# Kernel optimization log

Hardware: AMD Instinct MI355X
Metric: run time of the kernel (lower is better)

## Reference

```python
import jax, jax.numpy as jnp
import numpy as np

H, DK, NHID, L, G = 8, 32, 256, 2, 16
SQRT_DK = float(np.sqrt(DK))
N_IN = (3, 3, 2)  # number of etypes whose dst is word, topic, doc (for mean cross-reducer)


def _seg_softmax_agg(a, val, dst, n):
    # per-destination-node softmax over incoming edges (DGL mailbox softmax), then weighted sum
    m = jax.ops.segment_max(a, dst, num_segments=n)
    m = jnp.where(m < -1e30, 0.0, m)  # empty segments
    ex = jnp.exp(a - m[dst])
    den = jax.ops.segment_sum(ex, dst, num_segments=n)
    w = ex / jnp.maximum(den, 1e-9)[dst]
    return jax.ops.segment_sum(w[..., None] * val, dst, num_segments=n)  # [n,H,DK]


def _forward(word_id, topic_id, g_word, g_topic, g_doc,
             src_ww, dst_ww, src_wd, dst_wd, src_wt, dst_wt, src_td, dst_td, src_tt, dst_tt,
             time_ww, time_wd, time_wt, time_td, y_data,
             word_embeds, topic_embeds, doc_gen, adapt_w, adapt_b,
             time_tab, time_w, time_b,
             kW, kB, qW, qB, vW, vB, aW, aB, skip, ln_g, ln_b,
             pri, attR, msgR, out_w, out_b):
    nd = g_doc.shape[0]
    # initial node features: word via adapt_ws, topic lookup, doc broadcast
    h = [word_embeds[word_id] @ adapt_w + adapt_b,
         topic_embeds[topic_id],
         jnp.tile(doc_gen, (nd, 1))]
    te = lambda t: time_tab[t] @ time_w + time_b  # RelTemporalEncoding: lin(emb(t)) -> [E, DK]
    th_ww, th_wd, th_wt, th_td = te(time_ww), te(time_wd), te(time_wt), te(time_td)
    # etype index order: wt, wd, td, tt, ww, tw, dt, dw ; ntype index: 0=word,1=topic,2=doc
    rels = [(0, 0, 1, src_wt, dst_wt, th_wt), (1, 0, 2, src_wd, dst_wd, th_wd),
            (2, 1, 2, src_td, dst_td, th_td), (3, 1, 1, src_tt, dst_tt, None),
            (4, 0, 0, src_ww, dst_ww, th_ww), (5, 1, 0, dst_wt, src_wt, th_wt),
            (6, 2, 1, dst_td, src_td, th_td), (7, 2, 0, dst_wd, src_wd, th_wd)]
    for li in range(L):
        k = [(h[i] @ kW[li, i] + kB[li, i]).reshape(-1, H, DK) for i in range(3)]
        q = [(h[i] @ qW[li, i] + qB[li, i]).reshape(-1, H, DK) for i in range(3)]
        v = [(h[i] @ vW[li, i] + vB[li, i]).reshape(-1, H, DK) for i in range(3)]
        t = [jnp.zeros((h[i].shape[0], NHID), h[i].dtype) for i in range(3)]
        for (e, s, d, src, dst, th) in rels:
            key = jnp.einsum('ehk,hkl->ehl', k[s][src], attR[li, e])
            a = (q[d][dst] * key).sum(-1) * pri[li, e] / SQRT_DK  # [E,H]
            val = jnp.einsum('ehk,hkl->ehl', v[s][src], msgR[li, e])
            if th is not None:
                val = val + th[:, None, :]  # temporal encoding broadcast over heads
            n = h[d].shape[0]
            he = _seg_softmax_agg(a, val, dst, n)
            t[d] = t[d] + jax.nn.relu(he.reshape(n, NHID))  # relu per etype, then mean
        nh = []
        for i in range(3):
            alpha = jax.nn.sigmoid(skip[li, i])
            trans = (t[i] / N_IN[i]) @ aW[li, i] + aB[li, i]
            out = trans * alpha + h[i] * (1.0 - alpha)
            mu = out.mean(-1, keepdims=True)
            var = ((out - mu) ** 2).mean(-1, keepdims=True)
            nh.append((out - mu) / jnp.sqrt(var + 1e-5) * ln_g[li, i] + ln_b[li, i])
        h = nh
    gmax = lambda x, g: jax.ops.segment_max(x, g, num_segments=G)  # dgl.max_nodes
    gi = jnp.concatenate([gmax(h[2], g_doc), gmax(h[0], g_word), gmax(h[1], g_topic)], -1)
    logits = gi @ out_w + out_b  # [G,1]
    z = logits.reshape(-1)
    loss = jnp.mean(jnp.maximum(z, 0.0) - z * y_data + jnp.log1p(jnp.exp(-jnp.abs(z))))
    return loss, jax.nn.sigmoid(logits)


def setup_inputs():
    key = jax.random.key(0)
    ks = iter(jax.random.split(key, 80))
    nrm = lambda shape, s=0.05: jax.random.normal(next(ks), shape, jnp.float32) * s
    ri = lambda shape, hi: jax.random.randint(next(ks), shape, 0, hi)
    NW, NT, ND = 30000, 2000, 8000
    d = {}
    d['word_id'] = ri((NW,), 15000)
    d['topic_id'] = ri((NT,), 50)
    d['g_word'] = jnp.sort(ri((NW,), G))
    d['g_topic'] = jnp.sort(ri((NT,), G))
    d['g_doc'] = jnp.sort(ri((ND,), G))
    d['src_ww'] = ri((40000,), NW); d['dst_ww'] = ri((40000,), NW); d['time_ww'] = ri((40000,), 7)
    d['src_wd'] = ri((30000,), NW); d['dst_wd'] = ri((30000,), ND); d['time_wd'] = ri((30000,), 7)
    d['src_wt'] = ri((30000,), NW); d['dst_wt'] = ri((30000,), NT); d['time_wt'] = ri((30000,), 7)
    d['src_td'] = ri((25000,), NT); d['dst_td'] = ri((25000,), ND); d['time_td'] = ri((25000,), 7)
    d['src_tt'] = ri((20000,), NT); d['dst_tt'] = ri((20000,), NT)
    d['y_data'] = jax.random.uniform(next(ks), (G,), jnp.float32)
    d['word_embeds'] = nrm((15000, 256))
    d['topic_embeds'] = nrm((50, 256), 0.1)
    d['doc_gen'] = nrm((1, 256), 0.1)
    d['adapt_w'] = nrm((256, 256)); d['adapt_b'] = nrm((256,), 0.01)
    d['time_tab'] = nrm((7, 32), 0.1); d['time_w'] = nrm((32, 32), 0.1); d['time_b'] = nrm((32,), 0.01)
    for nm in ['kW', 'qW', 'vW', 'aW']:
        d[nm] = nrm((L, 3, 256, 256))
    for nm in ['kB', 'qB', 'vB', 'aB']:
        d[nm] = nrm((L, 3, 256), 0.01)
    d['skip'] = jnp.ones((L, 3))
    d['ln_g'] = jnp.ones((L, 3, 256)); d['ln_b'] = jnp.zeros((L, 3, 256))
    d['pri'] = jnp.ones((L, 8, H))
    d['attR'] = nrm((L, 8, H, DK, DK), 0.1)
    d['msgR'] = nrm((L, 8, H, DK, DK), 0.1)
    d['out_w'] = nrm((3 * NHID, 1)); d['out_b'] = jnp.zeros((1,))
    return d


def reference(word_id, topic_id, g_word, g_topic, g_doc,
              src_ww, dst_ww, time_ww, src_wd, dst_wd, time_wd,
              src_wt, dst_wt, time_wt, src_td, dst_td, time_td,
              src_tt, dst_tt, y_data,
              word_embeds, topic_embeds, doc_gen, adapt_w, adapt_b,
              time_tab, time_w, time_b,
              kW, kB, qW, qB, vW, vB, aW, aB, skip, ln_g, ln_b,
              pri, attR, msgR, out_w, out_b):
    return _forward(word_id, topic_id, g_word, g_topic, g_doc,
                    src_ww, dst_ww, src_wd, dst_wd, src_wt, dst_wt, src_td, dst_td, src_tt, dst_tt,
                    time_ww, time_wd, time_wt, time_td, y_data,
                    word_embeds, topic_embeds, doc_gen, adapt_w, adapt_b,
                    time_tab, time_w, time_b,
                    kW, kB, qW, qB, vW, vB, aW, aB, skip, ln_g, ln_b,
                    pri, attR, msgR, out_w, out_b)
```

## Files before the change

### kernel.cpp

```cpp
#include <hip/hip_runtime.h>
#include <hip/hip_bf16.h>
#include <math.h>

#define H 8
#define DK 32
#define NHID 256
#define LNUM 2
#define GNUM 16

typedef float f32x4 __attribute__((ext_vector_type(4)));
typedef short bf16x8 __attribute__((ext_vector_type(8)));
typedef unsigned short u16x8 __attribute__((ext_vector_type(8)));

__device__ __forceinline__ unsigned encf(float f) {
    unsigned u = __float_as_uint(f);
    return (u & 0x80000000u) ? ~u : (u | 0x80000000u);
}
__device__ __forceinline__ float decf(unsigned u) {
    return __uint_as_float((u & 0x80000000u) ? (u ^ 0x80000000u) : ~u);
}
__device__ __forceinline__ float bfd(unsigned short u) {
    return __uint_as_float(((unsigned)u) << 16);
}
__device__ __forceinline__ unsigned short f2bf(float x) {
    __hip_bfloat16 b = __float2bfloat16(x);
    return *reinterpret_cast<unsigned short*>(&b);
}

#define APAN2(row, kb) ((((kb) >> 7) << 12) + ((row) << 6) + ((((kb) & 127) ^ (((row) & 7) << 4)) >> 1))
__device__ __forceinline__ size_t swzA(int row, int col ) {
    return (((size_t)(row >> 6)) << 14) + (size_t)APAN2(row & 63, col * 2);
}
#define SWZB(row, kb)  (((row) << 6) + ((((kb) ^ (((row) & 7) << 4))) >> 1))

struct CsrArgs  { const int* dst[8]; const int* srcA[8]; const int* timA[8];
                  int relOfs[9]; int dstBase[8]; };
struct BdAllArgs{ int rows[8]; int srcOfs[8]; int outOfs[8]; };
struct Ek1PosArgs{ int kOfs[8]; int qOfs[8]; };
struct Ek3AllArgs{ int dstBase[8]; int vOfs[8]; int hasTim[8]; int typeRel[9]; int nrT[3];
                   int cumN[4]; int tOfs[3]; float oScale[3]; };
struct GmaxArgs { const float* hp[3]; const int* grp[3]; int n[3]; int colBase[3]; };
struct GBArgs   { int rb[4]; int nLoc[3]; int li3; };
struct MLArgs   { int rowOfs[4]; int nLoc[3]; int li3; };

__global__ void te_kernel(const float* __restrict__ time_tab, const float* __restrict__ time_w,
                          const float* __restrict__ time_b, float* __restrict__ te7) {
    int t = threadIdx.x >> 5, j = threadIdx.x & 31;
    if (t < 7) {
        float s = time_b[j];
        #pragma unroll
        for (int i = 0; i < 32; ++i) s += time_tab[t * 32 + i] * time_w[i * 32 + j];
        te7[t * 32 + j] = s;
    }
}

__global__ void gather_rows(const float* __restrict__ emb, const int* __restrict__ idx,
                            float* __restrict__ out, unsigned short* __restrict__ outB, int n) {
    int row = blockIdx.x, c = threadIdx.x;
    if (row < n) {
        float v = emb[(size_t)idx[row] * 256 + c];
        out[(size_t)row * 256 + c] = v;
        outB[swzA(row, c)] = f2bf(v);
    }
}

__global__ void bcast_row(const float* __restrict__ src, float* __restrict__ out,
                          unsigned short* __restrict__ outB, int n) {
    int row = blockIdx.x, c = threadIdx.x;
    if (row < n) {
        float v = src[c];
        out[(size_t)row * 256 + c] = v;
        outB[swzA(row, c)] = f2bf(v);
    }
}

__global__ __launch_bounds__(256) void wtr_kernel(
    const float* __restrict__ adaptW, const float* __restrict__ kW, const float* __restrict__ qW,
    const float* __restrict__ vW, const float* __restrict__ aW, unsigned short* __restrict__ WT) {
    int z = blockIdx.z;
    const float* src;
    if (z == 0) src = adaptW;
    else if (z < 7)  src = kW + (size_t)(z - 1) * 65536;
    else if (z < 13) src = qW + (size_t)(z - 7) * 65536;
    else if (z < 19) src = vW + (size_t)(z - 13) * 65536;
    else             src = aW + (size_t)(z - 19) * 65536;
    unsigned short* dst = WT + (size_t)z * 65536;
    __shared__ float tile[32][33];
    int tx = threadIdx.x & 31, ty = threadIdx.x >> 5;
    int kb = blockIdx.x * 32, cb = blockIdx.y * 32;
    #pragma unroll
    for (int i = 0; i < 4; ++i)
        tile[ty + i * 8][tx] = src[(size_t)(kb + ty + i * 8) * 256 + cb + tx];
    __syncthreads();
    #pragma unroll
    for (int i = 0; i < 4; ++i) {
        int col = cb + ty + i * 8, k = kb + tx;
        dst[((col >> 6) * 4 + (k >> 6)) * 4096 + SWZB(col & 63, (k & 63) * 2)] =
            f2bf(tile[tx][ty + i * 8]);
    }
}

__global__ __launch_bounds__(256) void gemm_batch(
    const unsigned short* __restrict__ Apan,
    const unsigned short* __restrict__ WT, int wBase, int nz,
    const float* __restrict__ b0, const float* __restrict__ b1, const float* __restrict__ b2,
    void* __restrict__ o0, void* __restrict__ o1, void* __restrict__ o2,
    int outBf16, GBArgs ga)
{
    __shared__ unsigned short As[64 * 256];
    __shared__ unsigned short Bs[2][4096];
    const int tid = threadIdx.x;
    const int lane = tid & 63, wv = tid >> 6;
    const int b = blockIdx.x;
    const int t = (b >= ga.rb[2]) ? 2 : ((b >= ga.rb[1]) ? 1 : 0);
    const int nLoc = ga.nLoc[t];
    const int locRowBase = (b - ga.rb[t]) * 64;
    const int cb6 = blockIdx.y;
    const int mBase = wBase + ga.li3 + t;
    {
        const u16x8* src = reinterpret_cast<const u16x8*>(Apan + (((size_t)b) << 14));
        u16x8* dst = reinterpret_cast<u16x8*>(As);
        #pragma unroll
        for (int it = 0; it < 8; ++it)
            dst[it * 256 + tid] = src[it * 256 + tid];
    }
    const int fr = lane & 15, fg = lane >> 4;
    const int wrow = (wv & 1) * 32, wcol = (wv >> 1) * 32;
    const int nt = nz * 4;
    {
        const u16x8* src = reinterpret_cast<const u16x8*>(WT + (size_t)mBase * 65536 + (size_t)(cb6 * 4 + 0) * 4096);
        u16x8* dst = reinterpret_cast<u16x8*>(Bs[0]);
        dst[tid] = src[tid];
        dst[tid + 256] = src[tid + 256];
    }
    __syncthreads();

    f32x4 acc[2][2];
    #pragma unroll
    for (int m = 0; m < 2; ++m)
        #pragma unroll
        for (int nn = 0; nn < 2; ++nn) acc[m][nn] = 0.f;

    for (int tt2 = 0; tt2 < nt; ++tt2) {
        const int cur = tt2 & 1;
        const int ks = tt2 & 3, z = tt2 >> 2;
        u16x8 w0, w1;
        const bool pf = (tt2 + 1 < nt);
        if (pf) {
            int tn = tt2 + 1;
            const u16x8* src = reinterpret_cast<const u16x8*>(
                WT + (size_t)(mBase + (tn >> 2) * 6) * 65536 + (size_t)(cb6 * 4 + (tn & 3)) * 4096);
            w0 = src[tid];
            w1 = src[tid + 256];
        }
        #pragma unroll
        for (int kk = 0; kk < 2; ++kk) {
            bf16x8 af0 = *reinterpret_cast<bf16x8*>(&As[APAN2(wrow + fr,      ks * 128 + kk * 64 + fg * 16)]);
            bf16x8 af1 = *reinterpret_cast<bf16x8*>(&As[APAN2(wrow + 16 + fr, ks * 128 + kk * 64 + fg * 16)]);
            bf16x8 bf0 = *reinterpret_cast<bf16x8*>(&Bs[cur][SWZB(wcol + fr,      kk * 64 + fg * 16)]);
            bf16x8 bf1 = *reinterpret_cast<bf16x8*>(&Bs[cur][SWZB(wcol + 16 + fr, kk * 64 + fg * 16)]);
            acc[0][0] = __builtin_amdgcn_mfma_f32_16x16x32_bf16(af0, bf0, acc[0][0], 0, 0, 0);
            acc[0][1] = __builtin_amdgcn_mfma_f32_16x16x32_bf16(af0, bf1, acc[0][1], 0, 0, 0);
            acc[1][0] = __builtin_amdgcn_mfma_f32_16x16x32_bf16(af1, bf0, acc[1][0], 0, 0, 0);
            acc[1][1] = __builtin_amdgcn_mfma_f32_16x16x32_bf16(af1, bf1, acc[1][1], 0, 0, 0);
        }
        if (pf) {
            u16x8* dst = reinterpret_cast<u16x8*>(Bs[cur ^ 1]);
            dst[tid] = w0;
            dst[tid + 256] = w1;
        }
        if (ks == 3) {
            const float* biasB = (z == 0) ? b0 : ((z == 1) ? b1 : b2);
            const float* bias = biasB + (size_t)(ga.li3 + t) * 256;
            void* outp = (z == 0) ? o0 : ((z == 1) ? o1 : o2);
            #pragma unroll
            for (int m = 0; m < 2; ++m) {
                #pragma unroll
                for (int r = 0; r < 4; ++r) {
                    int lr = locRowBase + wrow + m * 16 + fg * 4 + r;
                    if (lr >= nLoc) continue;
                    size_t gr = (size_t)b * 64 + wrow + m * 16 + fg * 4 + r;
                    #pragma unroll
                    for (int nn = 0; nn < 2; ++nn) {
                        int gc = cb6 * 64 + wcol + nn * 16 + fr;
                        float v = acc[m][nn][r] + bias[gc];
                        if (outBf16) ((unsigned short*)outp)[gr * 256 + gc] = f2bf(v);
                        else         ((float*)outp)[gr * 256 + gc] = v;
                    }
                }
            }
            #pragma unroll
            for (int m = 0; m < 2; ++m)
                #pragma unroll
                for (int nn = 0; nn < 2; ++nn) acc[m][nn] = 0.f;
        }
        __syncthreads();
    }
}

__global__ __launch_bounds__(256) void gemm_init(
    const float* __restrict__ A, const int* __restrict__ gidx,
    const unsigned short* __restrict__ WT, const float* __restrict__ bias,
    float* __restrict__ outF, unsigned short* __restrict__ dupB, int n)
{
    __shared__ unsigned short As[64 * 256];
    __shared__ unsigned short Bs[2][4096];
    const int tid = threadIdx.x;
    const int lane = tid & 63, wv = tid >> 6;
    const int rowBase = blockIdx.x * 64;
    const int cb6 = blockIdx.y;
    #pragma unroll 4
    for (int it = 0; it < 16; ++it) {
        int row = it * 4 + wv;
        int r = rowBase + row;
        ushort4 p = make_ushort4(0, 0, 0, 0);
        if (r < n) {
            int ar = gidx[r];
            float4 v = *reinterpret_cast<const float4*>(A + (size_t)ar * 256 + lane * 4);
            p.x = f2bf(v.x); p.y = f2bf(v.y); p.z = f2bf(v.z); p.w = f2bf(v.w);
        }
        *reinterpret_cast<ushort4*>(&As[APAN2(row, lane * 8)]) = p;
    }
    const int fr = lane & 15, fg = lane >> 4;
    const int wrow = (wv & 1) * 32, wcol = (wv >> 1) * 32;
    {
        const u16x8* src = reinterpret_cast<const u16x8*>(WT + (size_t)(cb6 * 4 + 0) * 4096);
        u16x8* dst = reinterpret_cast<u16x8*>(Bs[0]);
        dst[tid] = src[tid];
        dst[tid + 256] = src[tid + 256];
    }
    __syncthreads();
    f32x4 acc[2][2];
    #pragma unroll
    for (int m = 0; m < 2; ++m)
        #pragma unroll
        for (int nn = 0; nn < 2; ++nn) acc[m][nn] = 0.f;
    for (int t = 0; t < 4; ++t) {
        const int cur = t & 1;
        u16x8 w0, w1;
        const bool pf = (t + 1 < 4);
        if (pf) {
            const u16x8* src = reinterpret_cast<const u16x8*>(WT + (size_t)(cb6 * 4 + t + 1) * 4096);
            w0 = src[tid];
            w1 = src[tid + 256];
        }
        #pragma unroll
        for (int kk = 0; kk < 2; ++kk) {
            bf16x8 af0 = *reinterpret_cast<bf16x8*>(&As[APAN2(wrow + fr,      t * 128 + kk * 64 + fg * 16)]);
            bf16x8 af1 = *reinterpret_cast<bf16x8*>(&As[APAN2(wrow + 16 + fr, t * 128 + kk * 64 + fg * 16)]);
            bf16x8 bf0 = *reinterpret_cast<bf16x8*>(&Bs[cur][SWZB(wcol + fr,      kk * 64 + fg * 16)]);
            bf16x8 bf1 = *reinterpret_cast<bf16x8*>(&Bs[cur][SWZB(wcol + 16 + fr, kk * 64 + fg * 16)]);
            acc[0][0] = __builtin_amdgcn_mfma_f32_16x16x32_bf16(af0, bf0, acc[0][0], 0, 0, 0);
            acc[0][1] = __builtin_amdgcn_mfma_f32_16x16x32_bf16(af0, bf1, acc[0][1], 0, 0, 0);
            acc[1][0] = __builtin_amdgcn_mfma_f32_16x16x32_bf16(af1, bf0, acc[1][0], 0, 0, 0);
            acc[1][1] = __builtin_amdgcn_mfma_f32_16x16x32_bf16(af1, bf1, acc[1][1], 0, 0, 0);
        }
        if (pf) {
            u16x8* dst = reinterpret_cast<u16x8*>(Bs[cur ^ 1]);
            dst[tid] = w0;
            dst[tid + 256] = w1;
        }
        __syncthreads();
    }
    #pragma unroll
    for (int m = 0; m < 2; ++m) {
        #pragma unroll
        for (int r = 0; r < 4; ++r) {
            int gr = rowBase + wrow + m * 16 + fg * 4 + r;
            if (gr >= n) continue;
            #pragma unroll
            for (int nn = 0; nn < 2; ++nn) {
                int gc = cb6 * 64 + wcol + nn * 16 + fr;
                float v = acc[m][nn][r] + bias[gc];
                outF[(size_t)gr * 256 + gc] = v;
                dupB[swzA(gr, gc)] = f2bf(v);
            }
        }
    }
}

__global__ __launch_bounds__(256) void bd_all(
    const unsigned short* __restrict__ inPb, const float* __restrict__ Rl,
    const float* __restrict__ priL, int isV,
    unsigned short* __restrict__ outAll, BdAllArgs A)
{
    const int rel = blockIdx.z;
    const int n = A.rows[rel];
    const int rowBase = blockIdx.x * 128;
    if (rowBase >= n) return;
    const unsigned short* in = inPb + (size_t)A.srcOfs[rel] * 256;
    const float* R = Rl + (size_t)rel * 8192;
    unsigned short* out = outAll + (size_t)A.outOfs[rel] * 256;
    const int head = blockIdx.y;
    const float oscale = isV ? 1.f : (priL[rel * 8 + head] * 0.17677669529663687f);
    const int tid = threadIdx.x, lane = tid & 63, wv = tid >> 6;
    const int fr = lane & 15, fg = lane >> 4;
    const float* Rh = R + head * 1024;
    bf16x8 b0, b1;
    #pragma unroll
    for (int j = 0; j < 8; ++j) {
        b0[j] = (short)f2bf(Rh[(fg * 8 + j) * 32 + fr] * oscale);
        b1[j] = (short)f2bf(Rh[(fg * 8 + j) * 32 + 16 + fr] * oscale);
    }
    const int r0 = rowBase + wv * 32 + fr;
    const int r1 = r0 + 16;
    const int rc0 = (r0 < n) ? r0 : n - 1;
    const int rc1 = (r1 < n) ? r1 : n - 1;
    bf16x8 a0 = *reinterpret_cast<const bf16x8*>(in + (size_t)rc0 * 256 + head * 32 + fg * 8);
    bf16x8 a1 = *reinterpret_cast<const bf16x8*>(in + (size_t)rc1 * 256 + head * 32 + fg * 8);
    f32x4 acc00 = 0.f, acc01 = 0.f, acc10 = 0.f, acc11 = 0.f;
    acc00 = __builtin_amdgcn_mfma_f32_16x16x32_bf16(a0, b0, acc00, 0, 0, 0);
    acc01 = __builtin_amdgcn_mfma_f32_16x16x32_bf16(a0, b1, acc01, 0, 0, 0);
    acc10 = __builtin_amdgcn_mfma_f32_16x16x32_bf16(a1, b0, acc10, 0, 0, 0);
    acc11 = __builtin_amdgcn_mfma_f32_16x16x32_bf16(a1, b1, acc11, 0, 0, 0);
    const int colB = head * 32 + fr;
    #pragma unroll
    for (int r = 0; r < 4; ++r) {
        int g0 = rowBase + wv * 32 + fg * 4 + r;
        if (g0 < n) {
            out[(size_t)g0 * 256 + colB]      = f2bf(acc00[r]);
            out[(size_t)g0 * 256 + colB + 16] = f2bf(acc01[r]);
        }
        int g1 = g0 + 16;
        if (g1 < n) {
            out[(size_t)g1 * 256 + colB]      = f2bf(acc10[r]);
            out[(size_t)g1 * 256 + colB + 16] = f2bf(acc11[r]);
        }
    }
}

__global__ __launch_bounds__(256) void ek1_pos(
    const unsigned short* __restrict__ qPb, const unsigned short* __restrict__ kattAll,
    const int* __restrict__ payload, const int* __restrict__ drel,
    float* __restrict__ alogC, Ek1PosArgs A, int totE)
{
    int gid = blockIdx.x * 256 + threadIdx.x;
    int p = gid >> 3, h = gid & 7;
    if (p >= totE) return;
    int dr = drel[p];
    int d = dr & 0xFFFFF, rel = dr >> 20;
    int s = payload[p] & 0xFFFF;
    const u16x8* q8 = reinterpret_cast<const u16x8*>(qPb + ((size_t)(A.qOfs[rel] + d)) * 256 + h * 32);
    const u16x8* k8 = reinterpret_cast<const u16x8*>(kattAll + ((size_t)(A.kOfs[rel] + s)) * 256 + h * 32);
    float a = 0.f;
    #pragma unroll
    for (int j = 0; j < 4; ++j) {
        u16x8 qv = q8[j], kv = k8[j];
        #pragma unroll
        for (int m = 0; m < 8; ++m) a += bfd(qv[m]) * bfd(kv[m]);
    }
    alogC[(size_t)p * 8 + h] = a;
}

__global__ __launch_bounds__(256) void ek3_all(
    const unsigned short* __restrict__ vmsgAll, const float* __restrict__ alogC,
    const int* __restrict__ rowptrAll, const int* __restrict__ payload,
    const float* __restrict__ te7, unsigned short* __restrict__ tB, Ek3AllArgs A)
{
    __shared__ float sTe[224];
    if (threadIdx.x < 224) sTe[threadIdx.x] = te7[threadIdx.x];
    __syncthreads();
    int wv = threadIdx.x >> 6, lane = threadIdx.x & 63;
    int dg = blockIdx.x * 4 + wv;
    if (dg >= A.cumN[3]) return;
    const int ty = (dg >= A.cumN[2]) ? 2 : ((dg >= A.cumN[1]) ? 1 : 0);
    const int d = dg - A.cumN[ty];
    const int bl = lane >> 3, hl = lane & 7;
    const int c = lane * 4, hq = lane >> 3;
    float t0 = 0.f, t1 = 0.f, t2 = 0.f, t3 = 0.f;
    const int nr = A.nrT[ty];
    for (int j = 0; j < nr; ++j) {
        const int rel = A.typeRel[ty * 3 + j];
        int base = A.dstBase[rel] + d;
        int beg = rowptrAll[base], end = rowptrAll[base + 1];
        if (beg == end) continue;
        const int useTim = A.hasTim[rel];
        int rO = A.vOfs[rel];
        float m = -INFINITY, den = 0.f;
        float a0 = 0.f, a1 = 0.f, a2 = 0.f, a3 = 0.f;
        for (int p0 = beg; p0 < end; p0 += 8) {
            int p = p0 + bl;
            bool valid = p < end;
            int pc = valid ? p : end - 1;
            float a = valid ? alogC[(size_t)pc * 8 + hl] : -INFINITY;
            int pk = payload[pc];
            int sS = pk & 0xFFFF, tT = pk >> 16;
            float bm = a;
            bm = fmaxf(bm, __shfl_xor(bm, 8));
            bm = fmaxf(bm, __shfl_xor(bm, 16));
            bm = fmaxf(bm, __shfl_xor(bm, 32));
            float bmA = __shfl(bm, hq);
            float mN = fmaxf(m, bmA);
            float sc = __expf(m - mN);
            den *= sc; a0 *= sc; a1 *= sc; a2 *= sc; a3 *= sc;
            m = mN;
            float mL = __shfl(mN, hl * 8);
            float ex = valid ? __expf(a - mL) : 0.f;
            float ds = ex;
            ds += __shfl_xor(ds, 8);
            ds += __shfl_xor(ds, 16);
            ds += __shfl_xor(ds, 32);
            den += __shfl(ds, hq);
            int nb = end - p0; if (nb > 8) nb = 8;
            for (int b = 0; b < nb; ++b) {
                float w = __shfl(ex, b * 8 + hq);
                int sB = __shfl(sS, b * 8);
                ushort4 v = *reinterpret_cast<const ushort4*>(vmsgAll + ((size_t)(rO + sB)) * 256 + c);
                float vx = bfd(v.x), vy = bfd(v.y), vz = bfd(v.z), vw = bfd(v.w);
                if (useTim) {
                    int tBt = __shfl(tT, b * 8);
                    const float* tp = &sTe[tBt * 32 + (c & 31)];
                    vx += tp[0]; vy += tp[1]; vz += tp[2]; vw += tp[3];
                }
                a0 += w * vx; a1 += w * vy; a2 += w * vz; a3 += w * vw;
            }
        }
        float inv = 1.f / fmaxf(den, 1e-9f);
        t0 += fmaxf(a0 * inv, 0.f); t1 += fmaxf(a1 * inv, 0.f);
        t2 += fmaxf(a2 * inv, 0.f); t3 += fmaxf(a3 * inv, 0.f);
    }
    float os = A.oScale[ty];
    ushort4 o;
    o.x = f2bf(t0 * os); o.y = f2bf(t1 * os);
    o.z = f2bf(t2 * os); o.w = f2bf(t3 * os);
    *reinterpret_cast<ushort4*>(tB + swzA(A.tOfs[ty] + d, c)) = o;
}

__global__ void count_all(CsrArgs A, int* __restrict__ cnt, int totE) {
    int gid = blockIdx.x * 256 + threadIdx.x;
    if (gid >= totE) return;
    int r = 0;
    while (gid >= A.relOfs[r + 1]) ++r;
    int e = gid - A.relOfs[r];
    atomicAdd(&cnt[A.dstBase[r] + A.dst[r][e]], 1);
}
__global__ __launch_bounds__(1024) void scan1_k(const int* __restrict__ cnt, int* __restrict__ part,
                                                int* __restrict__ bsum, int n) {
    __shared__ int buf[1024];
    int tid = threadIdx.x, gid = blockIdx.x * 1024 + tid;
    int x = (gid < n) ? cnt[gid] : 0;
    buf[tid] = x; __syncthreads();
    for (int off = 1; off < 1024; off <<= 1) {
        int y = (tid >= off) ? buf[tid - off] : 0;
        __syncthreads();
        buf[tid] += y;
        __syncthreads();
    }
    if (gid < n) part[gid] = buf[tid];
    if (tid == 1023) bsum[blockIdx.x] = buf[1023];
}
__global__ __launch_bounds__(256) void scan2_k(int* __restrict__ bsum, int nb) {
    __shared__ int buf[256];
    int tid = threadIdx.x;
    buf[tid] = (tid < nb) ? bsum[tid] : 0;
    __syncthreads();
    for (int off = 1; off < 256; off <<= 1) {
        int y = (tid >= off) ? buf[tid - off] : 0;
        __syncthreads();
        buf[tid] += y;
        __syncthreads();
    }
    if (tid < nb) bsum[tid] = buf[tid];
}
__global__ void scan3_k(const int* __restrict__ cnt, const int* __restrict__ part,
                        const int* __restrict__ bsum, int* __restrict__ rowptr,
                        int* __restrict__ cur, int n) {
    int gid = blockIdx.x * 256 + threadIdx.x;
    if (gid < n) {
        int b = gid >> 10;
        int add = (b > 0) ? bsum[b - 1] : 0;
        int inc = part[gid] + add;
        rowptr[gid + 1] = inc;
        cur[gid] = inc - cnt[gid];
    }
    if (gid == 0) rowptr[0] = 0;
}
__global__ void scatter_all(CsrArgs A, int* __restrict__ cur,
                            int* __restrict__ payload, int* __restrict__ drel, int totE) {
    int gid = blockIdx.x * 256 + threadIdx.x;
    if (gid >= totE) return;
    int r = 0;
    while (gid >= A.relOfs[r + 1]) ++r;
    int e = gid - A.relOfs[r];
    int d = A.dst[r][e];
    int p = atomicAdd(&cur[A.dstBase[r] + d], 1);
    int s = A.srcA[r][e];
    int t = A.timA[r] ? A.timA[r][e] : 0;
    payload[p] = s | (t << 16);
    drel[p] = d | (r << 20);
}

__global__ __launch_bounds__(256) void mix_ln_all(
    float* __restrict__ h, unsigned short* __restrict__ hB, const float* __restrict__ trans,
    const float* __restrict__ skipP, const float* __restrict__ g, const float* __restrict__ b,
    MLArgs M)
{
    int row = blockIdx.x;
    int t = (row >= M.rowOfs[2]) ? 2 : ((row >= M.rowOfs[1]) ? 1 : 0);
    int d = row - M.rowOfs[t];
    if (d >= M.nLoc[t]) return;
    int j = M.li3 + t;
    int c = threadIdx.x;
    float alpha = 1.f / (1.f + expf(-skipP[j]));
    size_t off = (size_t)row * 256 + c;
    float o = trans[off] * alpha + h[off] * (1.f - alpha);
    float s = o, ss = o * o;
    #pragma unroll
    for (int dd = 1; dd < 64; dd <<= 1) { s += __shfl_xor(s, dd); ss += __shfl_xor(ss, dd); }
    __shared__ float rS[4], rSS[4];
    int w = threadIdx.x >> 6, lane = threadIdx.x & 63;
    if (lane == 0) { rS[w] = s; rSS[w] = ss; }
    __syncthreads();
    float S = rS[0] + rS[1] + rS[2] + rS[3];
    float SS = rSS[0] + rSS[1] + rSS[2] + rSS[3];
    float mean = S * (1.f / 256.f);
    float var = fmaxf(SS * (1.f / 256.f) - mean * mean, 0.f);
    float rs = rsqrtf(var + 1e-5f);
    float v = (o - mean) * rs * g[(size_t)j * 256 + c] + b[(size_t)j * 256 + c];
    h[off] = v;
    hB[swzA(row, c)] = f2bf(v);
}

__global__ __launch_bounds__(256) void gmax_all(GmaxArgs A, unsigned* __restrict__ gi) {
    int ty = blockIdx.y;
    int n = A.n[ty];
    int r0 = blockIdx.x * 64;
    if (r0 >= n) return;
    int col = threadIdx.x;
    const float* hp = A.hp[ty];
    const int* grp = A.grp[ty];
    int cbase = A.colBase[ty];
    int rend = (r0 + 64 < n) ? r0 + 64 : n;
    int cur = grp[r0];
    float m = -INFINITY;
    for (int r = r0; r < rend; ++r) {
        int g = grp[r];
        if (g != cur) {
            atomicMax(&gi[cur * 768 + cbase + col], encf(m));
            cur = g; m = -INFINITY;
        }
        m = fmaxf(m, hp[(size_t)r * 256 + col]);
    }
    atomicMax(&gi[cur * 768 + cbase + col], encf(m));
}

__global__ void gi_init(unsigned* __restrict__ gi) {
    int i = blockIdx.x * 256 + threadIdx.x;
    if (i < 16 * 768) gi[i] = 0x007FFFFFu;
}

__global__ __launch_bounds__(1024) void final_k(const unsigned* __restrict__ gi,
                                                const float* __restrict__ out_w,
                                                const float* __restrict__ out_b,
                                                const float* __restrict__ y,
                                                float* __restrict__ out) {
    int w = threadIdx.x >> 6, lane = threadIdx.x & 63;
    float s = 0.f;
    for (int c = lane; c < 768; c += 64) s += decf(gi[w * 768 + c]) * out_w[c];
    #pragma unroll
    for (int d = 1; d < 64; d <<= 1) s += __shfl_xor(s, d);
    __shared__ float lloss[16];
    if (lane == 0) {
        float z = s + out_b[0];
        out[1 + w] = 1.f / (1.f + expf(-z));
        lloss[w] = fmaxf(z, 0.f) - z * y[w] + log1pf(expf(-fabsf(z)));
    }
    __syncthreads();
    if (threadIdx.x == 0) {
        float L = 0.f;
        for (int g2 = 0; g2 < 16; ++g2) L += lloss[g2];
        out[0] = L * (1.f / 16.f);
    }
}

extern "C" void kernel_launch(void* const* d_in, const int* in_sizes, int n_in,
                              void* d_out, int out_size, void* d_ws, size_t ws_size,
                              hipStream_t stream) {
    const int* word_id   = (const int*)d_in[0];
    const int* topic_id  = (const int*)d_in[1];
    const int* g_word    = (const int*)d_in[2];
    const int* g_topic   = (const int*)d_in[3];
    const int* g_doc     = (const int*)d_in[4];
    const int* src_ww = (const int*)d_in[5];  const int* dst_ww = (const int*)d_in[6];  const int* time_ww = (const int*)d_in[7];
    const int* src_wd = (const int*)d_in[8];  const int* dst_wd = (const int*)d_in[9];  const int* time_wd = (const int*)d_in[10];
    const int* src_wt = (const int*)d_in[11]; const int* dst_wt = (const int*)d_in[12]; const int* time_wt = (const int*)d_in[13];
    const int* src_td = (const int*)d_in[14]; const int* dst_td = (const int*)d_in[15]; const int* time_td = (const int*)d_in[16];
    const int* src_tt = (const int*)d_in[17]; const int* dst_tt = (const int*)d_in[18];
    const float* y_data      = (const float*)d_in[19];
    const float* word_embeds = (const float*)d_in[20];
    const float* topic_embeds= (const float*)d_in[21];
    const float* doc_gen     = (const float*)d_in[22];
    const float* adapt_w     = (const float*)d_in[23];
    const float* adapt_b     = (const float*)d_in[24];
    const float* time_tab    = (const float*)d_in[25];
    const float* time_w      = (const float*)d_in[26];
    const float* time_b      = (const float*)d_in[27];
    const float* kW = (const float*)d_in[28];
    const float* qW = (const float*)d_in[29];
    const float* vW = (const float*)d_in[30];
    const float* aW = (const float*)d_in[31];
    const float* kB = (const float*)d_in[32];
    const float* qB = (const float*)d_in[33];
    const float* vB = (const float*)d_in[34];
    const float* aB = (const float*)d_in[35];
    const float* skip = (const float*)d_in[36];
    const float* ln_g = (const float*)d_in[37];
    const float* ln_b = (const float*)d_in[38];
    const float* pri  = (const float*)d_in[39];
    const float* attR = (const float*)d_in[40];
    const float* msgR = (const float*)d_in[41];
    const float* out_w = (const float*)d_in[42];
    const float* out_b = (const float*)d_in[43];

    const int NW = in_sizes[0], NT = in_sizes[1], ND = in_sizes[4];
    const int E_ww = in_sizes[5], E_wd = in_sizes[8], E_wt = in_sizes[11],
              E_td = in_sizes[14], E_tt = in_sizes[17];
    const int nN[3] = {NW, NT, ND};
    const float invNin[3] = {1.f / 3.f, 1.f / 3.f, 1.f / 2.f};

    struct Rel { int e, s, d; const int* src; const int* dst; const int* tim; int E; };
    const Rel rels[8] = {
        {0, 0, 1, src_wt, dst_wt, time_wt, E_wt},
        {1, 0, 2, src_wd, dst_wd, time_wd, E_wd},
        {2, 1, 2, src_td, dst_td, time_td, E_td},
        {3, 1, 1, src_tt, dst_tt, nullptr, E_tt},
        {4, 0, 0, src_ww, dst_ww, time_ww, E_ww},
        {5, 1, 0, dst_wt, src_wt, time_wt, E_wt},
        {6, 2, 1, dst_td, src_td, time_td, E_td},
        {7, 2, 0, dst_wd, src_wd, time_wd, E_wd},
    };

    int relOfs[9]; relOfs[0] = 0;
    int dstBase[8]; int acc = 0;
    for (int r = 0; r < 8; ++r) { relOfs[r + 1] = relOfs[r] + rels[r].E; dstBase[r] = acc; acc += nN[rels[r].d]; }
    const int totE = relOfs[8], totD = acc;

    int relRowOfs[8], relRowsTot = 0, maxRelRows = 0;
    for (int r = 0; r < 8; ++r) {
        relRowOfs[r] = relRowsTot;
        relRowsTot += nN[rels[r].s];
        if (nN[rels[r].s] > maxRelRows) maxRelRows = nN[rels[r].s];
    }

    int nPad[3], rowOfsT[4];
    rowOfsT[0] = 0;
    for (int i = 0; i < 3; ++i) { nPad[i] = (nN[i] + 63) & ~63; rowOfsT[i + 1] = rowOfsT[i] + nPad[i]; }
    const int totPad = rowOfsT[3];

    float* base = (float*)d_ws;
    size_t off = 0;
    auto take = [&](size_t nElems) { float* p = base + off; off += (nElems + 63) & ~(size_t)63; return p; };
    float* hPbase = take((size_t)totPad * 256);
    unsigned short* hB = (unsigned short*)take((size_t)totPad * 128);
    unsigned short* tB = (unsigned short*)take((size_t)totPad * 128);
    unsigned short* kPb = (unsigned short*)take((size_t)totPad * 128);
    unsigned short* qPb = (unsigned short*)take((size_t)totPad * 128);
    unsigned short* vPb = (unsigned short*)take((size_t)totPad * 128);
    size_t arenaFloats = (size_t)relRowsTot * 128;
    if ((size_t)totPad * 256 > arenaFloats) arenaFloats = (size_t)totPad * 256;
    float* uni = take(arenaFloats);
    unsigned short* arena = (unsigned short*)uni;
    float* trans = uni;
    unsigned short* WT = (unsigned short*)take((size_t)25 * 32768);
    float* alogC = take((size_t)totE * 8);
    float* te7  = take(7 * 32);
    unsigned* gi = (unsigned*)take(16 * 768);
    int* cntAll = (int*)take(totD);
    int* part   = (int*)take(totD);
    int* bsum   = (int*)take(256);
    int* rowptrAll = (int*)take(totD + 1);
    int* curAll = (int*)take(totD);
    int* payload = (int*)take(totE);
    int* drel    = (int*)take(totE);
    (void)ws_size; (void)n_in; (void)out_size;

    te_kernel<<<1, 256, 0, stream>>>(time_tab, time_w, time_b, te7);
    {
        dim3 g(8, 8, 25);
        wtr_kernel<<<g, 256, 0, stream>>>(adapt_w, kW, qW, vW, aW, WT);
    }
    CsrArgs ca;
    for (int r = 0; r < 8; ++r) {
        ca.dst[r] = rels[r].dst; ca.srcA[r] = rels[r].src; ca.timA[r] = rels[r].tim;
        ca.dstBase[r] = dstBase[r];
    }
    for (int r = 0; r < 9; ++r) ca.relOfs[r] = relOfs[r];
    hipMemsetAsync(cntAll, 0, (size_t)totD * sizeof(int), stream);
    count_all<<<(totE + 255) / 256, 256, 0, stream>>>(ca, cntAll, totE);
    int nb = (totD + 1023) / 1024;
    scan1_k<<<nb, 1024, 0, stream>>>(cntAll, part, bsum, totD);
    scan2_k<<<1, 256, 0, stream>>>(bsum, nb);
    scan3_k<<<(totD + 255) / 256, 256, 0, stream>>>(cntAll, part, bsum, rowptrAll, curAll, totD);
    scatter_all<<<(totE + 255) / 256, 256, 0, stream>>>(ca, curAll, payload, drel, totE);
    gi_init<<<48, 256, 0, stream>>>(gi);

    {
        dim3 g((NW + 63) / 64, 4);
        gemm_init<<<g, 256, 0, stream>>>(word_embeds, word_id, WT, adapt_b, hPbase, hB, NW);
    }
    gather_rows<<<NT, 256, 0, stream>>>(topic_embeds, topic_id,
                                        hPbase + (size_t)rowOfsT[1] * 256,
                                        hB + (size_t)rowOfsT[1] * 256, NT);
    bcast_row<<<ND, 256, 0, stream>>>(doc_gen,
                                      hPbase + (size_t)rowOfsT[2] * 256,
                                      hB + (size_t)rowOfsT[2] * 256, ND);

    BdAllArgs ba;
    Ek1PosArgs e1;
    Ek3AllArgs e3;
    for (int r = 0; r < 8; ++r) {
        const Rel& R = rels[r];
        ba.rows[r] = nN[R.s];
        ba.srcOfs[r] = rowOfsT[R.s];
        ba.outOfs[r] = relRowOfs[r];
        e1.kOfs[r] = relRowOfs[r]; e1.qOfs[r] = rowOfsT[R.d];
        e3.dstBase[r] = dstBase[r]; e3.vOfs[r] = relRowOfs[r];
        e3.hasTim[r] = (R.tim != nullptr) ? 1 : 0;
    }
    const int typeRel[9] = {4, 5, 7, 0, 3, 6, 1, 2, 0};
    for (int i = 0; i < 9; ++i) e3.typeRel[i] = typeRel[i];
    e3.nrT[0] = 3; e3.nrT[1] = 3; e3.nrT[2] = 2;
    e3.cumN[0] = 0; e3.cumN[1] = NW; e3.cumN[2] = NW + NT; e3.cumN[3] = NW + NT + ND;
    for (int i = 0; i < 3; ++i) { e3.tOfs[i] = rowOfsT[i]; e3.oScale[i] = invNin[i]; }

    GBArgs gb;
    for (int i = 0; i < 4; ++i) gb.rb[i] = rowOfsT[i] / 64;
    for (int i = 0; i < 3; ++i) gb.nLoc[i] = nN[i];
    MLArgs ml;
    for (int i = 0; i < 4; ++i) ml.rowOfs[i] = rowOfsT[i];
    for (int i = 0; i < 3; ++i) ml.nLoc[i] = nN[i];

    const int totBlocks = totPad / 64;
    const int totD3 = NW + NT + ND;
    for (int li = 0; li < LNUM; ++li) {
        gb.li3 = li * 3; ml.li3 = li * 3;
        {
            dim3 g(totBlocks, 4);
            gemm_batch<<<g, 256, 0, stream>>>(hB, WT, 1, 3, kB, qB, vB,
                                              kPb, qPb, vPb, 1, gb);
        }
        {
            dim3 g((maxRelRows + 127) / 128, 8, 8);
            bd_all<<<g, 256, 0, stream>>>(kPb, attR + (size_t)li * 8 * 8192,
                                          pri + (size_t)li * 8 * 8, 0, arena, ba);
        }
        ek1_pos<<<((size_t)totE * 8 + 255) / 256, 256, 0, stream>>>(
            qPb, arena, payload, drel, alogC, e1, totE);
        {
            dim3 g((maxRelRows + 127) / 128, 8, 8);
            bd_all<<<g, 256, 0, stream>>>(vPb, msgR + (size_t)li * 8 * 8192,
                                          pri + (size_t)li * 8 * 8, 1, arena, ba);
        }
        ek3_all<<<(totD3 + 3) / 4, 256, 0, stream>>>(arena, alogC, rowptrAll, payload,
                                                     te7, tB, e3);
        {
            dim3 g(totBlocks, 4);
            gemm_batch<<<g, 256, 0, stream>>>(tB, WT, 19, 1, aB, aB, aB,
                                              trans, trans, trans, 0, gb);
        }
        mix_ln_all<<<totPad, 256, 0, stream>>>(hPbase, hB, trans, skip, ln_g, ln_b, ml);
    }

    GmaxArgs ga;
    ga.hp[0] = hPbase + (size_t)rowOfsT[2] * 256; ga.grp[0] = g_doc;   ga.n[0] = ND; ga.colBase[0] = 0;
    ga.hp[1] = hPbase;                             ga.grp[1] = g_word;  ga.n[1] = NW; ga.colBase[1] = 256;
    ga.hp[2] = hPbase + (size_t)rowOfsT[1] * 256; ga.grp[2] = g_topic; ga.n[2] = NT; ga.colBase[2] = 512;
    int maxN = NW > ND ? (NW > NT ? NW : NT) : (ND > NT ? ND : NT);
    dim3 gg((maxN + 63) / 64, 3);
    gmax_all<<<gg, 256, 0, stream>>>(ga, gi);
    final_k<<<1, 1024, 0, stream>>>(gi, out_w, out_b, y_data, (float*)d_out);
}
```

Baseline: 658.2 us.

## Split edge softmax normalization into separate pass before message aggregation

Adds a kernel that computes per-destination, per-head softmax max and denominator over incoming edges and rewrites the attention logits in place as normalized weights. The aggregation kernel then just takes a weighted sum of messages, with no online-softmax rescaling or shuffle reductions inside its edge loop. The aim is to shorten the latency-bound gather loop, at the price of an extra launch and a second read-modify-write pass over the logits.

```diff
diff --git a/kernel.cpp b/kernel.cpp
--- a/kernel.cpp
+++ b/kernel.cpp
@@ -37,6 +37,7 @@
                   int relOfs[9]; int dstBase[8]; };
 struct BdAllArgs{ int rows[8]; int srcOfs[8]; int outOfs[8]; };
 struct Ek1PosArgs{ int kOfs[8]; int qOfs[8]; };
+struct EkwArgs  { int dstBase[8]; int typeRel[9]; int nrT[3]; int cumN[4]; };
 struct Ek3AllArgs{ int dstBase[8]; int vOfs[8]; int hasTim[8]; int typeRel[9]; int nrT[3];
                    int cumN[4]; int tOfs[3]; float oScale[3]; };
 struct GmaxArgs { const float* hp[3]; const int* grp[3]; int n[3]; int colBase[3]; };
@@ -352,6 +353,52 @@
     alogC[(size_t)p * 8 + h] = a;
 }
 
+__global__ __launch_bounds__(256) void ekw_all(
+    float* __restrict__ alogC, const int* __restrict__ rowptrAll, EkwArgs A)
+{
+    int wv = threadIdx.x >> 6, lane = threadIdx.x & 63;
+    int dg = blockIdx.x * 4 + wv;
+    if (dg >= A.cumN[3]) return;
+    const int ty = (dg >= A.cumN[2]) ? 2 : ((dg >= A.cumN[1]) ? 1 : 0);
+    const int d = dg - A.cumN[ty];
+    const int bl = lane >> 3, hl = lane & 7;
+    const int nr = A.nrT[ty];
+    for (int j = 0; j < nr; ++j) {
+        const int rel = A.typeRel[ty * 3 + j];
+        int base = A.dstBase[rel] + d;
+        int beg = rowptrAll[base], end = rowptrAll[base + 1];
+        if (beg == end) continue;
+        float m = -INFINITY, den = 0.f;
+        for (int p0 = beg; p0 < end; p0 += 8) {
+            int p = p0 + bl;
+            bool valid = p < end;
+            float a = valid ? alogC[(size_t)(valid ? p : end - 1) * 8 + hl] : -INFINITY;
+            float bm = a;
+            bm = fmaxf(bm, __shfl_xor(bm, 8));
+            bm = fmaxf(bm, __shfl_xor(bm, 16));
+            bm = fmaxf(bm, __shfl_xor(bm, 32));
+            float mN = fmaxf(m, bm);
+            float sc = __expf(m - mN);
+            den *= sc;
+            float ex = valid ? __expf(a - mN) : 0.f;
+            float ds = ex;
+            ds += __shfl_xor(ds, 8);
+            ds += __shfl_xor(ds, 16);
+            ds += __shfl_xor(ds, 32);
+            den += ds;
+            m = mN;
+        }
+        float inv = 1.f / fmaxf(den, 1e-9f);
+        for (int p0 = beg; p0 < end; p0 += 8) {
+            int p = p0 + bl;
+            if (p < end) {
+                float a = alogC[(size_t)p * 8 + hl];
+                alogC[(size_t)p * 8 + hl] = __expf(a - m) * inv;
+            }
+        }
+    }
+}
+
 __global__ __launch_bounds__(256) void ek3_all(
     const unsigned short* __restrict__ vmsgAll, const float* __restrict__ alogC,
     const int* __restrict__ rowptrAll, const int* __restrict__ payload,
@@ -376,34 +423,17 @@
         if (beg == end) continue;
         const int useTim = A.hasTim[rel];
         int rO = A.vOfs[rel];
-        float m = -INFINITY, den = 0.f;
         float a0 = 0.f, a1 = 0.f, a2 = 0.f, a3 = 0.f;
         for (int p0 = beg; p0 < end; p0 += 8) {
             int p = p0 + bl;
             bool valid = p < end;
             int pc = valid ? p : end - 1;
-            float a = valid ? alogC[(size_t)pc * 8 + hl] : -INFINITY;
+            float w8 = valid ? alogC[(size_t)pc * 8 + hl] : 0.f;
             int pk = payload[pc];
             int sS = pk & 0xFFFF, tT = pk >> 16;
-            float bm = a;
-            bm = fmaxf(bm, __shfl_xor(bm, 8));
-            bm = fmaxf(bm, __shfl_xor(bm, 16));
-            bm = fmaxf(bm, __shfl_xor(bm, 32));
-            float bmA = __shfl(bm, hq);
-            float mN = fmaxf(m, bmA);
-            float sc = __expf(m - mN);
-            den *= sc; a0 *= sc; a1 *= sc; a2 *= sc; a3 *= sc;
-            m = mN;
-            float mL = __shfl(mN, hl * 8);
-            float ex = valid ? __expf(a - mL) : 0.f;
-            float ds = ex;
-            ds += __shfl_xor(ds, 8);
-            ds += __shfl_xor(ds, 16);
-            ds += __shfl_xor(ds, 32);
-            den += __shfl(ds, hq);
             int nb = end - p0; if (nb > 8) nb = 8;
             for (int b = 0; b < nb; ++b) {
-                float w = __shfl(ex, b * 8 + hq);
+                float w = __shfl(w8, b * 8 + hq);
                 int sB = __shfl(sS, b * 8);
                 ushort4 v = *reinterpret_cast<const ushort4*>(vmsgAll + ((size_t)(rO + sB)) * 256 + c);
                 float vx = bfd(v.x), vy = bfd(v.y), vz = bfd(v.z), vw = bfd(v.w);
@@ -415,9 +445,8 @@
                 a0 += w * vx; a1 += w * vy; a2 += w * vz; a3 += w * vw;
             }
         }
-        float inv = 1.f / fmaxf(den, 1e-9f);
-        t0 += fmaxf(a0 * inv, 0.f); t1 += fmaxf(a1 * inv, 0.f);
-        t2 += fmaxf(a2 * inv, 0.f); t3 += fmaxf(a3 * inv, 0.f);
+        t0 += fmaxf(a0, 0.f); t1 += fmaxf(a1, 0.f);
+        t2 += fmaxf(a2, 0.f); t3 += fmaxf(a3, 0.f);
     }
     float os = A.oScale[ty];
     ushort4 o;
@@ -707,6 +736,7 @@
 
     BdAllArgs ba;
     Ek1PosArgs e1;
+    EkwArgs ew;
     Ek3AllArgs e3;
     for (int r = 0; r < 8; ++r) {
         const Rel& R = rels[r];
@@ -714,12 +744,15 @@
         ba.srcOfs[r] = rowOfsT[R.s];
         ba.outOfs[r] = relRowOfs[r];
         e1.kOfs[r] = relRowOfs[r]; e1.qOfs[r] = rowOfsT[R.d];
+        ew.dstBase[r] = dstBase[r];
         e3.dstBase[r] = dstBase[r]; e3.vOfs[r] = relRowOfs[r];
         e3.hasTim[r] = (R.tim != nullptr) ? 1 : 0;
     }
     const int typeRel[9] = {4, 5, 7, 0, 3, 6, 1, 2, 0};
-    for (int i = 0; i < 9; ++i) e3.typeRel[i] = typeRel[i];
+    for (int i = 0; i < 9; ++i) { ew.typeRel[i] = typeRel[i]; e3.typeRel[i] = typeRel[i]; }
+    ew.nrT[0] = 3; ew.nrT[1] = 3; ew.nrT[2] = 2;
     e3.nrT[0] = 3; e3.nrT[1] = 3; e3.nrT[2] = 2;
+    ew.cumN[0] = 0; ew.cumN[1] = NW; ew.cumN[2] = NW + NT; ew.cumN[3] = NW + NT + ND;
     e3.cumN[0] = 0; e3.cumN[1] = NW; e3.cumN[2] = NW + NT; e3.cumN[3] = NW + NT + ND;
     for (int i = 0; i < 3; ++i) { e3.tOfs[i] = rowOfsT[i]; e3.oScale[i] = invNin[i]; }
 
@@ -746,6 +779,7 @@
         }
         ek1_pos<<<((size_t)totE * 8 + 255) / 256, 256, 0, stream>>>(
             qPb, arena, payload, drel, alogC, e1, totE);
+        ekw_all<<<(totD3 + 3) / 4, 256, 0, stream>>>(alogC, rowptrAll, ew);
         {
             dim3 g((maxRelRows + 127) / 128, 8, 8);
             bd_all<<<g, 256, 0, stream>>>(vPb, msgR + (size_t)li * 8 * 8192,
```

Result: slower. 701.1 us (+6.5%).
